# Kernel tuning notes

Hardware: AMD Instinct MI355X
Metric: run time of the kernel (lower is better)

The kernel has to match this reference:

```python
import jax, jax.numpy as jnp
import numpy as np

WIN = 7
NUM_HEADS = 4
DIM = 128
HEAD_DIM = DIM // NUM_HEADS
N = WIN * WIN
NW = 1024   # windows per image (224/7)^2
B_ = 16384  # batch(16) * NW


def _pos_index(win):
    # Swin relative-position index, static int table [N, N]
    coords = np.stack(np.meshgrid(np.arange(win), np.arange(win), indexing='ij'))
    cf = coords.reshape(2, -1)                       # [2, N]
    rel = cf[:, :, None] - cf[:, None, :]            # [2, N, N]
    rel = rel.transpose(1, 2, 0).astype(np.int64)    # [N, N, 2]
    rel[:, :, 0] += win - 1
    rel[:, :, 1] += win - 1
    rel[:, :, 0] *= 2 * win - 1
    return rel.sum(-1)                               # [N, N]

POS_INDEX = jnp.asarray(_pos_index(WIN))


def setup_inputs() -> dict:
    key = jax.random.key(0)
    ks = jax.random.split(key, 11)
    s = 0.02
    return {
        'x': jax.random.normal(ks[0], (B_, N, DIM), jnp.float32),
        'mask': jax.random.normal(ks[1], (NW, N, N), jnp.float32),
        'Wq': jax.random.normal(ks[2], (DIM, DIM), jnp.float32) * s,
        'bq': jax.random.normal(ks[3], (DIM,), jnp.float32) * s,
        'Wk': jax.random.normal(ks[4], (DIM, DIM), jnp.float32) * s,
        'bk': jax.random.normal(ks[5], (DIM,), jnp.float32) * s,
        'Wv': jax.random.normal(ks[6], (DIM, DIM), jnp.float32) * s,
        'bv': jax.random.normal(ks[7], (DIM,), jnp.float32) * s,
        'Wproj': jax.random.normal(ks[8], (DIM, DIM), jnp.float32) * s,
        'bproj': jax.random.normal(ks[9], (DIM,), jnp.float32) * s,
        'rel_bias': jax.random.normal(ks[10], ((2 * WIN - 1) ** 2, NUM_HEADS), jnp.float32) * s,
    }


def reference(x, mask, Wq, bq, Wk, bk, Wv, bv, Wproj, bproj, rel_bias):
    Bw, n, C = x.shape
    H, hd = NUM_HEADS, HEAD_DIM
    scale = hd ** -0.5

    def heads(t):  # [B, N, C] -> [B, H, N, hd]
        return t.reshape(Bw, n, H, hd).transpose(0, 2, 1, 3)

    q = heads(x @ Wq.T + bq) * scale
    k = heads(x @ Wk.T + bk)
    v = heads(x @ Wv.T + bv)

    attn = jnp.einsum('bhnd,bhmd->bhnm', q, k)              # [B, H, N, N]
    rb = rel_bias[POS_INDEX.reshape(-1)].reshape(n, n, H)    # [N, N, H]
    attn = attn + rb.transpose(2, 0, 1)[None]                # + [1, H, N, N]

    nw = mask.shape[0]
    attn = attn.reshape(Bw // nw, nw, H, n, n) + mask[None, :, None]
    attn = attn.reshape(Bw, H, n, n)

    attn = jax.nn.softmax(attn, axis=-1)
    out = jnp.einsum('bhnm,bhmd->bhnd', attn, v)             # [B, H, N, hd]
    out = out.transpose(0, 2, 1, 3).reshape(Bw, n, C)
    return out @ Wproj.T + bproj
```

## Files before the change

### kernel.cpp

```cpp
#include <hip/hip_runtime.h>
#include <hip/hip_bf16.h>
#include <stdint.h>

#define NTOK 49
#define LOG2E 1.4426950408889634f
#define SCALE2 0.25507662683243807f

typedef __attribute__((ext_vector_type(4))) float f32x4;
typedef __attribute__((ext_vector_type(2))) unsigned int u32x2;
typedef __attribute__((ext_vector_type(4))) unsigned int u32x4;
typedef __attribute__((ext_vector_type(8))) short bfrag;
typedef __attribute__((ext_vector_type(4))) short s16x4;
typedef __attribute__((ext_vector_type(4))) float facc;

#define MFMA16(A,B,C) __builtin_amdgcn_mfma_f32_16x16x32_bf16(A,B,C,0,0,0)
#define EXP2(x) __builtin_amdgcn_exp2f(x)

__device__ __forceinline__ unsigned pk2bf(float a, float b) {
    unsigned r;
    asm("v_cvt_pk_bf16_f32 %0, %1, %2" : "=v"(r) : "v"(a), "v"(b));
    return r;
}
__device__ __forceinline__ short f2bf(float a) {
    unsigned ua = __builtin_bit_cast(unsigned, a);
    ua = ua + 0x7fffu + ((ua >> 16) & 1u);
    return (short)(ua >> 16);
}
__device__ __forceinline__ float bf2f(short s) {
    unsigned u = ((unsigned)(unsigned short)s) << 16;
    return __builtin_bit_cast(float, u);
}
__device__ __forceinline__ int sw256(int row, int cb) { return row * 256 + (cb ^ ((row & 7) << 4)); }
__device__ __forceinline__ int sw128(int row, int cb) { return row * 128 + (cb ^ ((row & 7) << 4)); }

__global__ void prep_w(const float* __restrict__ Wq, const float* __restrict__ Wk,
                       const float* __restrict__ Wv, const float* __restrict__ Wp,
                       const float* __restrict__ relb, short* __restrict__ ws)
{
    int t = blockIdx.x * 256 + threadIdx.x;
    if (t >= 16384) return;
    int e = t & 7, lane = (t >> 3) & 63, ks = (t >> 9) & 3, tile = t >> 11;
    int row = tile * 16 + (lane & 15);
    int col = ks * 32 + (lane >> 4) * 8 + e;
    int src = row * 128 + col;
    ws[t]         = f2bf(Wq[src]);
    ws[16384 + t] = f2bf(Wk[src]);
    ws[32768 + t] = f2bf(Wv[src]);
    ws[49152 + t] = f2bf(Wp[src]);
    int e2 = t & 3, lane2 = (t >> 2) & 63, mt = (t >> 8) & 3, rt = (t >> 10) & 3, h = t >> 12;
    int r = rt * 16 + (lane2 & 15);
    int m = mt * 16 + (lane2 >> 4) * 4 + e2;
    float v = 0.f;
    if (r < NTOK && m < NTOK) {
        int idx = ((r / 7 - m / 7) + 6) * 13 + ((r % 7) - (m % 7) + 6);
        v = relb[idx * 4 + h] * LOG2E;
    }
    ws[65536 + t] = f2bf(v);
}

__global__ void prep_cmb(const float* __restrict__ mask, const float* __restrict__ relb,
                         short* __restrict__ cmb)
{
    int t = blockIdx.x * 256 + threadIdx.x;
    int e = t & 3, lane = (t >> 2) & 63, mt = (t >> 8) & 3, rt = (t >> 10) & 3;
    int h = (t >> 12) & 3, w = t >> 14;
    int r = rt * 16 + (lane & 15);
    int m = mt * 16 + (lane >> 4) * 4 + e;
    float v = -1e30f;
    if (r < NTOK && m < NTOK) {
        int idx = ((r / 7 - m / 7) + 6) * 13 + ((r % 7) - (m % 7) + 6);
        v = (mask[w * (NTOK * NTOK) + r * NTOK + m] + relb[idx * 4 + h]) * LOG2E;
    }
    cmb[t] = f2bf(v);
}

__device__ __forceinline__ char* pstrip(char* smem_, int wid, int r, int mb) {
    return smem_ + ((mb >> 6) << 14) + r * 256 + ((wid * 64 + (mb & 63)) ^ ((r & 7) << 4));
}

__global__ __launch_bounds__(256, 2) void swin_fwd_p(
    const float* __restrict__ x,
    const float* __restrict__ bq, const float* __restrict__ bk,
    const float* __restrict__ bv, const float* __restrict__ bp,
    const short* __restrict__ wqf, const short* __restrict__ wkf,
    const short* __restrict__ wvf, const short* __restrict__ wpf,
    const short* __restrict__ cmbf, float* __restrict__ out)
{
    extern __shared__ char smem[];
    char* qbuf  = smem;
    char* kbuf  = smem + 16384;
    char* vtbuf = smem + 32768;
    char* r4    = smem + 49152;

    const int b = blockIdx.x;
    const int tid = threadIdx.x;
    const int wid = tid >> 6;
    const int lane = tid & 63;
    const int l16 = lane & 15;
    const int lg = lane >> 4;

    float bqv[2][4], bkv[2][4], bpv[2][4], bvv2[2];
    #pragma unroll
    for (int mt = 0; mt < 2; ++mt) {
        #pragma unroll
        for (int j = 0; j < 4; ++j) {
            int o = wid * 32 + mt * 16 + lg * 4 + j;
            bqv[mt][j] = bq[o]; bkv[mt][j] = bk[o]; bpv[mt][j] = bp[o];
        }
        bvv2[mt] = bv[wid * 32 + mt * 16 + l16];
    }

    bfrag aq[2][4], ak[2][4], av[2][4];
    {
        const short* wq_i = wqf; const short* wk_i = wkf; const short* wv_i = wvf;
        asm volatile("" : "+s"(wq_i), "+s"(wk_i), "+s"(wv_i));
        #pragma unroll
        for (int mt = 0; mt < 2; ++mt)
            #pragma unroll
            for (int ks = 0; ks < 4; ++ks) {
                int fi = (((wid * 2 + mt) * 4 + ks) * 64 + lane) * 8;
                aq[mt][ks] = *(const bfrag*)(wq_i + fi);
                ak[mt][ks] = *(const bfrag*)(wk_i + fi);
                av[mt][ks] = *(const bfrag*)(wv_i + fi);
            }
    }

    f32x4 xr[7];
    {
        const float* xw0 = x + (size_t)b * 6272;
        #pragma unroll
        for (int ii = 0; ii < 7; ++ii) {
            int i4 = ii * 256 + tid;
            if (i4 < 1568) xr[ii] = *(const f32x4*)(xw0 + i4 * 4);
        }
        #pragma unroll
        for (int ii = 0; ii < 7; ++ii) {
            int i4 = ii * 256 + tid;
            if (i4 < 1568) {
                int tok = i4 >> 5, col = (i4 & 31) * 4;
                u32x2 w; w.x = pk2bf(xr[ii].x, xr[ii].y); w.y = pk2bf(xr[ii].z, xr[ii].w);
                *(u32x2*)(r4 + sw256(tok, col * 2)) = w;
            }
        }
        if (tid < 240) { u32x4 z = {0, 0, 0, 0}; *(u32x4*)(r4 + 49 * 256 + tid * 16) = z; }
    }
    __syncthreads();

    #pragma unroll 1
    for (int it = 0; it < 32; ++it) {
        const int win = b + (it << 9);

        {
            const float* xn = x + (size_t)((win + 512) & 16383) * 6272;
            #pragma unroll
            for (int ii = 0; ii < 7; ++ii) {
                int i4 = ii * 256 + tid;
                if (i4 < 1568) xr[ii] = *(const f32x4*)(xn + i4 * 4);
            }
        }

        {
            #pragma unroll
            for (int nt = 0; nt < 4; ++nt) {
                bfrag bx[4];
                #pragma unroll
                for (int ks = 0; ks < 4; ++ks)
                    bx[ks] = *(const bfrag*)(r4 + sw256(nt * 16 + l16, (ks * 32 + lg * 8) * 2));
                facc accq[2] = {{0,0,0,0},{0,0,0,0}};
                facc acck[2] = {{0,0,0,0},{0,0,0,0}};
                facc accv[2] = {{0,0,0,0},{0,0,0,0}};
                __builtin_amdgcn_s_setprio(1);
                #pragma unroll
                for (int ks = 0; ks < 4; ++ks)
                    #pragma unroll
                    for (int mt = 0; mt < 2; ++mt) {
                        accq[mt] = MFMA16(aq[mt][ks], bx[ks], accq[mt]);
                        acck[mt] = MFMA16(ak[mt][ks], bx[ks], acck[mt]);
                        accv[mt] = MFMA16(bx[ks], av[mt][ks], accv[mt]);
                    }
                __builtin_amdgcn_s_setprio(0);
                int tok = nt * 16 + l16;
                #pragma unroll
                for (int mt = 0; mt < 2; ++mt) {
                    int o0 = wid * 32 + mt * 16 + lg * 4;
                    u32x2 wq2, wk2, wv2;
                    wq2.x = pk2bf((accq[mt][0] + bqv[mt][0]) * SCALE2, (accq[mt][1] + bqv[mt][1]) * SCALE2);
                    wq2.y = pk2bf((accq[mt][2] + bqv[mt][2]) * SCALE2, (accq[mt][3] + bqv[mt][3]) * SCALE2);
                    wk2.x = pk2bf(acck[mt][0] + bkv[mt][0], acck[mt][1] + bkv[mt][1]);
                    wk2.y = pk2bf(acck[mt][2] + bkv[mt][2], acck[mt][3] + bkv[mt][3]);
                    *(u32x2*)(qbuf + sw256(tok, o0 * 2)) = wq2;
                    *(u32x2*)(kbuf + sw256(tok, o0 * 2)) = wk2;
                    wv2.x = pk2bf(accv[mt][0] + bvv2[mt], accv[mt][1] + bvv2[mt]);
                    wv2.y = pk2bf(accv[mt][2] + bvv2[mt], accv[mt][3] + bvv2[mt]);
                    *(u32x2*)(vtbuf + sw128(wid * 32 + mt * 16 + l16, (nt * 16 + lg * 4) * 2)) = wv2;
                }
            }
        }

        facc s[4][4];
        {
            bfrag ka[4], qb[4];
            int cb = (wid * 32 + lg * 8) * 2;
            #pragma unroll
            for (int t = 0; t < 4; ++t) {
                ka[t] = *(const bfrag*)(kbuf + sw256(t * 16 + l16, cb));
                qb[t] = *(const bfrag*)(qbuf + sw256(t * 16 + l16, cb));
            }
            __builtin_amdgcn_s_setprio(1);
            #pragma unroll
            for (int mt = 0; mt < 4; ++mt)
                #pragma unroll
                for (int rt = 0; rt < 4; ++rt) {
                    facc z = {0, 0, 0, 0};
                    s[mt][rt] = MFMA16(ka[mt], qb[rt], z);
                }
            __builtin_amdgcn_s_setprio(0);
        }
        __syncthreads();

        {
            #pragma unroll
            for (int ii = 0; ii < 7; ++ii) {
                int i4 = ii * 256 + tid;
                if (i4 < 1568) {
                    int tok = i4 >> 5, col = (i4 & 31) * 4;
                    u32x2 w; w.x = pk2bf(xr[ii].x, xr[ii].y); w.y = pk2bf(xr[ii].z, xr[ii].w);
                    *(u32x2*)(r4 + sw256(tok, col * 2)) = w;
                }
            }
        }

        float rs4[4];
        {
            const short* cw = cmbf + ((size_t)((win & 1023) * 4 + wid) << 12);
            #pragma unroll
            for (int rt = 0; rt < 4; ++rt) {
                float lgt[4][4];
                float mx = -3e38f;
                #pragma unroll
                for (int mt = 0; mt < 4; ++mt) {
                    s16x4 b4 = *(const s16x4*)(cw + ((rt * 4 + mt) << 8) + lane * 4);
                    #pragma unroll
                    for (int j = 0; j < 4; ++j) {
                        float v = s[mt][rt][j] + bf2f(b4[j]);
                        lgt[mt][j] = v;
                        mx = fmaxf(mx, v);
                    }
                }
                mx = fmaxf(mx, __shfl_xor(mx, 16));
                mx = fmaxf(mx, __shfl_xor(mx, 32));
                float sum = 0.f;
                u32x2 pw[4];
                #pragma unroll
                for (int mt = 0; mt < 4; ++mt) {
                    float p0 = EXP2(lgt[mt][0] - mx);
                    float p1 = EXP2(lgt[mt][1] - mx);
                    float p2 = EXP2(lgt[mt][2] - mx);
                    float p3 = EXP2(lgt[mt][3] - mx);
                    sum += (p0 + p1) + (p2 + p3);
                    pw[mt].x = pk2bf(p0, p1);
                    pw[mt].y = pk2bf(p2, p3);
                }
                sum += __shfl_xor(sum, 16);
                sum += __shfl_xor(sum, 32);
                rs4[rt] = __builtin_amdgcn_rcpf(sum);
                int r = rt * 16 + l16;
                #pragma unroll
                for (int mt = 0; mt < 4; ++mt)
                    *(u32x2*)pstrip(smem, wid, r, mt * 32 + lg * 8) = pw[mt];
            }
        }

        facc o2[2][4];
        {
            #pragma unroll
            for (int ct = 0; ct < 2; ++ct)
                #pragma unroll
                for (int rt = 0; rt < 4; ++rt) o2[ct][rt] = (facc){0, 0, 0, 0};
            #pragma unroll
            for (int ks = 0; ks < 2; ++ks) {
                bfrag avf[2], pb[4];
                #pragma unroll
                for (int ct = 0; ct < 2; ++ct)
                    avf[ct] = *(const bfrag*)(vtbuf + sw128(wid * 32 + ct * 16 + l16, (ks * 32 + lg * 8) * 2));
                #pragma unroll
                for (int rt = 0; rt < 4; ++rt)
                    pb[rt] = *(const bfrag*)pstrip(smem, wid, rt * 16 + l16, ks * 64 + lg * 16);
                __builtin_amdgcn_s_setprio(1);
                #pragma unroll
                for (int ct = 0; ct < 2; ++ct)
                    #pragma unroll
                    for (int rt = 0; rt < 4; ++rt)
                        o2[ct][rt] = MFMA16(avf[ct], pb[rt], o2[ct][rt]);
                __builtin_amdgcn_s_setprio(0);
            }
        }
        bfrag ap[2][4];
        {
            const short* wp_i = wpf;
            asm volatile("" : "+s"(wp_i));
            #pragma unroll
            for (int mt = 0; mt < 2; ++mt)
                #pragma unroll
                for (int ks = 0; ks < 4; ++ks)
                    ap[mt][ks] = *(const bfrag*)(wp_i + (((wid * 2 + mt) * 4 + ks) * 64 + lane) * 8);
        }
        __syncthreads();
        {
            #pragma unroll
            for (int ct = 0; ct < 2; ++ct) {
                int c0 = wid * 32 + ct * 16 + lg * 4;
                #pragma unroll
                for (int rt = 0; rt < 4; ++rt) {
                    int r = rt * 16 + l16;
                    float sc = rs4[rt];
                    u32x2 w;
                    w.x = pk2bf(o2[ct][rt][0] * sc, o2[ct][rt][1] * sc);
                    w.y = pk2bf(o2[ct][rt][2] * sc, o2[ct][rt][3] * sc);
                    *(u32x2*)(qbuf + sw256(r, c0 * 2)) = w;
                }
            }
        }
        __syncthreads();

        {
            facc acco[2][4];
            #pragma unroll
            for (int mt = 0; mt < 2; ++mt)
                #pragma unroll
                for (int tt = 0; tt < 4; ++tt) acco[mt][tt] = (facc){0, 0, 0, 0};
            #pragma unroll
            for (int tt = 0; tt < 4; ++tt) {
                bfrag ba[4];
                #pragma unroll
                for (int ks = 0; ks < 4; ++ks)
                    ba[ks] = *(const bfrag*)(qbuf + sw256(tt * 16 + l16, (ks * 32 + lg * 8) * 2));
                __builtin_amdgcn_s_setprio(1);
                #pragma unroll
                for (int ks = 0; ks < 4; ++ks)
                    #pragma unroll
                    for (int mt = 0; mt < 2; ++mt)
                        acco[mt][tt] = MFMA16(ap[mt][ks], ba[ks], acco[mt][tt]);
                __builtin_amdgcn_s_setprio(0);
            }
            float* ow = out + (size_t)win * 6272;
            #pragma unroll
            for (int tt = 0; tt < 4; ++tt) {
                int tok = tt * 16 + l16;
                if (tok < NTOK) {
                    #pragma unroll
                    for (int mt = 0; mt < 2; ++mt) {
                        int o0 = wid * 32 + mt * 16 + lg * 4;
                        f32x4 w;
                        w.x = acco[mt][tt][0] + bpv[mt][0];
                        w.y = acco[mt][tt][1] + bpv[mt][1];
                        w.z = acco[mt][tt][2] + bpv[mt][2];
                        w.w = acco[mt][tt][3] + bpv[mt][3];
                        *(f32x4*)(ow + tok * 128 + o0) = w;
                    }
                }
            }
        }

        {
            const short* wq_i = wqf; const short* wk_i = wkf; const short* wv_i = wvf;
            asm volatile("" : "+s"(wq_i), "+s"(wk_i), "+s"(wv_i));
            #pragma unroll
            for (int mt = 0; mt < 2; ++mt)
                #pragma unroll
                for (int ks = 0; ks < 4; ++ks) {
                    int fi = (((wid * 2 + mt) * 4 + ks) * 64 + lane) * 8;
                    aq[mt][ks] = *(const bfrag*)(wq_i + fi);
                    ak[mt][ks] = *(const bfrag*)(wk_i + fi);
                    av[mt][ks] = *(const bfrag*)(wv_i + fi);
                }
        }
        __syncthreads();
    }
}

__global__ __launch_bounds__(256, 2) void swin_fwd_fb(
    const float* __restrict__ x, const float* __restrict__ mask,
    const float* __restrict__ bq, const float* __restrict__ bk,
    const float* __restrict__ bv, const float* __restrict__ bp,
    const short* __restrict__ wqf, const short* __restrict__ wkf,
    const short* __restrict__ wvf, const short* __restrict__ wpf,
    const short* __restrict__ rbf, float* __restrict__ out)
{
    extern __shared__ char smem[];
    char* qbuf  = smem;
    char* kbuf  = smem + 16384;
    char* vtbuf = smem + 32768;
    char* r4    = smem + 49152;

    const int win = blockIdx.x;
    const int tid = threadIdx.x;
    const int wid = tid >> 6;
    const int lane = tid & 63;
    const int l16 = lane & 15;
    const int lg = lane >> 4;

    {
        const float* xw = x + (size_t)win * 6272;
        #pragma unroll
        for (int i = 0; i < 7; ++i) {
            int i4 = i * 256 + tid;
            if (i4 < 1568) {
                f32x4 f = *(const f32x4*)(xw + i4 * 4);
                int tok = i4 >> 5, col = (i4 & 31) * 4;
                u32x2 w; w.x = pk2bf(f.x, f.y); w.y = pk2bf(f.z, f.w);
                *(u32x2*)(r4 + sw256(tok, col * 2)) = w;
            }
        }
        if (tid < 240) { u32x4 z = {0, 0, 0, 0}; *(u32x4*)(r4 + 49 * 256 + tid * 16) = z; }
    }
    bfrag aq[2][4], ak[2][4], av[2][4];
    float bqv[2][4], bkv[2][4], bvv2[2];
    #pragma unroll
    for (int mt = 0; mt < 2; ++mt) {
        #pragma unroll
        for (int ks = 0; ks < 4; ++ks) {
            int fi = (((wid * 2 + mt) * 4 + ks) * 64 + lane) * 8;
            aq[mt][ks] = *(const bfrag*)(wqf + fi);
            ak[mt][ks] = *(const bfrag*)(wkf + fi);
            av[mt][ks] = *(const bfrag*)(wvf + fi);
        }
        #pragma unroll
        for (int j = 0; j < 4; ++j) {
            int o = wid * 32 + mt * 16 + lg * 4 + j;
            bqv[mt][j] = bq[o]; bkv[mt][j] = bk[o];
        }
        bvv2[mt] = bv[wid * 32 + mt * 16 + l16];
    }
    __syncthreads();

    {
        #pragma unroll
        for (int nt = 0; nt < 4; ++nt) {
            bfrag bx[4];
            #pragma unroll
            for (int ks = 0; ks < 4; ++ks)
                bx[ks] = *(const bfrag*)(r4 + sw256(nt * 16 + l16, (ks * 32 + lg * 8) * 2));
            facc accq[2] = {{0,0,0,0},{0,0,0,0}};
            facc acck[2] = {{0,0,0,0},{0,0,0,0}};
            facc accv[2] = {{0,0,0,0},{0,0,0,0}};
            #pragma unroll
            for (int ks = 0; ks < 4; ++ks)
                #pragma unroll
                for (int mt = 0; mt < 2; ++mt) {
                    accq[mt] = MFMA16(aq[mt][ks], bx[ks], accq[mt]);
                    acck[mt] = MFMA16(ak[mt][ks], bx[ks], acck[mt]);
                    accv[mt] = MFMA16(bx[ks], av[mt][ks], accv[mt]);
                }
            int tok = nt * 16 + l16;
            #pragma unroll
            for (int mt = 0; mt < 2; ++mt) {
                int o0 = wid * 32 + mt * 16 + lg * 4;
                u32x2 wq2, wk2, wv2;
                wq2.x = pk2bf((accq[mt][0] + bqv[mt][0]) * SCALE2, (accq[mt][1] + bqv[mt][1]) * SCALE2);
                wq2.y = pk2bf((accq[mt][2] + bqv[mt][2]) * SCALE2, (accq[mt][3] + bqv[mt][3]) * SCALE2);
                wk2.x = pk2bf(acck[mt][0] + bkv[mt][0], acck[mt][1] + bkv[mt][1]);
                wk2.y = pk2bf(acck[mt][2] + bkv[mt][2], acck[mt][3] + bkv[mt][3]);
                *(u32x2*)(qbuf + sw256(tok, o0 * 2)) = wq2;
                *(u32x2*)(kbuf + sw256(tok, o0 * 2)) = wk2;
                wv2.x = pk2bf(accv[mt][0] + bvv2[mt], accv[mt][1] + bvv2[mt]);
                wv2.y = pk2bf(accv[mt][2] + bvv2[mt], accv[mt][3] + bvv2[mt]);
                *(u32x2*)(vtbuf + sw128(wid * 32 + mt * 16 + l16, (nt * 16 + lg * 4) * 2)) = wv2;
            }
        }
    }
    facc s[4][4];
    {
        bfrag ka[4], qb[4];
        int cb = (wid * 32 + lg * 8) * 2;
        #pragma unroll
        for (int t = 0; t < 4; ++t) {
            ka[t] = *(const bfrag*)(kbuf + sw256(t * 16 + l16, cb));
            qb[t] = *(const bfrag*)(qbuf + sw256(t * 16 + l16, cb));
        }
        #pragma unroll
        for (int mt = 0; mt < 4; ++mt)
            #pragma unroll
            for (int rt = 0; rt < 4; ++rt) {
                facc z = {0, 0, 0, 0};
                s[mt][rt] = MFMA16(ka[mt], qb[rt], z);
            }
    }
    __syncthreads();
    {
        const float* mw = mask + (size_t)(win & 1023) * (NTOK * NTOK);
        #pragma unroll
        for (int i = 0; i < 16; ++i) {
            int flat = i * 256 + tid;
            int r = flat >> 6, m = flat & 63;
            float v = -1e30f;
            if (r < NTOK && m < NTOK) v = mw[r * 49 + m] * LOG2E;
            *(float*)(r4 + sw256(r, m * 4)) = v;
        }
    }
    __syncthreads();
    float rs4[4];
    {
        #pragma unroll
        for (int rt = 0; rt < 4; ++rt) {
            int r = rt * 16 + l16;
            float lgt[4][4];
            float mx = -3e38f;
            #pragma unroll
            for (int mt = 0; mt < 4; ++mt) {
                s16x4 b4 = *(const s16x4*)(rbf + ((wid * 16 + rt * 4 + mt) * 64 + lane) * 4);
                f32x4 mk = *(const f32x4*)(r4 + sw256(r, (mt * 16 + lg * 4) * 4));
                #pragma unroll
                for (int j = 0; j < 4; ++j) {
                    float v = s[mt][rt][j] + bf2f(b4[j]) + mk[j];
                    lgt[mt][j] = v;
                    mx = fmaxf(mx, v);
                }
            }
            mx = fmaxf(mx, __shfl_xor(mx, 16));
            mx = fmaxf(mx, __shfl_xor(mx, 32));
            float sum = 0.f;
            u32x2 pw[4];
            #pragma unroll
            for (int mt = 0; mt < 4; ++mt) {
                float p0 = EXP2(lgt[mt][0] - mx);
                float p1 = EXP2(lgt[mt][1] - mx);
                float p2 = EXP2(lgt[mt][2] - mx);
                float p3 = EXP2(lgt[mt][3] - mx);
                sum += (p0 + p1) + (p2 + p3);
                pw[mt].x = pk2bf(p0, p1);
                pw[mt].y = pk2bf(p2, p3);
            }
            sum += __shfl_xor(sum, 16);
            sum += __shfl_xor(sum, 32);
            rs4[rt] = __builtin_amdgcn_rcpf(sum);
            #pragma unroll
            for (int mt = 0; mt < 4; ++mt)
                *(u32x2*)pstrip(smem, wid, r, mt * 32 + lg * 8) = pw[mt];
        }
    }
    facc o2[2][4];
    {
        #pragma unroll
        for (int ct = 0; ct < 2; ++ct)
            #pragma unroll
            for (int rt = 0; rt < 4; ++rt) o2[ct][rt] = (facc){0, 0, 0, 0};
        #pragma unroll
        for (int ks = 0; ks < 2; ++ks) {
            bfrag avf[2], pb[4];
            #pragma unroll
            for (int ct = 0; ct < 2; ++ct)
                avf[ct] = *(const bfrag*)(vtbuf + sw128(wid * 32 + ct * 16 + l16, (ks * 32 + lg * 8) * 2));
            #pragma unroll
            for (int rt = 0; rt < 4; ++rt)
                pb[rt] = *(const bfrag*)pstrip(smem, wid, rt * 16 + l16, ks * 64 + lg * 16);
            #pragma unroll
            for (int ct = 0; ct < 2; ++ct)
                #pragma unroll
                for (int rt = 0; rt < 4; ++rt)
                    o2[ct][rt] = MFMA16(avf[ct], pb[rt], o2[ct][rt]);
        }
    }
    bfrag ap[2][4];
    float bpv[2][4];
    #pragma unroll
    for (int mt = 0; mt < 2; ++mt) {
        #pragma unroll
        for (int ks = 0; ks < 4; ++ks)
            ap[mt][ks] = *(const bfrag*)(wpf + (((wid * 2 + mt) * 4 + ks) * 64 + lane) * 8);
        #pragma unroll
        for (int j = 0; j < 4; ++j)
            bpv[mt][j] = bp[wid * 32 + mt * 16 + lg * 4 + j];
    }
    __syncthreads();
    {
        #pragma unroll
        for (int ct = 0; ct < 2; ++ct) {
            int c0 = wid * 32 + ct * 16 + lg * 4;
            #pragma unroll
            for (int rt = 0; rt < 4; ++rt) {
                int r = rt * 16 + l16;
                float sc = rs4[rt];
                u32x2 w;
                w.x = pk2bf(o2[ct][rt][0] * sc, o2[ct][rt][1] * sc);
                w.y = pk2bf(o2[ct][rt][2] * sc, o2[ct][rt][3] * sc);
                *(u32x2*)(r4 + sw256(r, c0 * 2)) = w;
            }
        }
    }
    __syncthreads();
    {
        facc acco[2][4];
        #pragma unroll
        for (int mt = 0; mt < 2; ++mt)
            #pragma unroll
            for (int tt = 0; tt < 4; ++tt) acco[mt][tt] = (facc){0, 0, 0, 0};
        #pragma unroll
        for (int tt = 0; tt < 4; ++tt) {
            bfrag ba[4];
            #pragma unroll
            for (int ks = 0; ks < 4; ++ks)
                ba[ks] = *(const bfrag*)(r4 + sw256(tt * 16 + l16, (ks * 32 + lg * 8) * 2));
            #pragma unroll
            for (int ks = 0; ks < 4; ++ks)
                #pragma unroll
                for (int mt = 0; mt < 2; ++mt)
                    acco[mt][tt] = MFMA16(ap[mt][ks], ba[ks], acco[mt][tt]);
        }
        float* ow = out + (size_t)win * 6272;
        #pragma unroll
        for (int tt = 0; tt < 4; ++tt) {
            int tok = tt * 16 + l16;
            if (tok < NTOK) {
                #pragma unroll
                for (int mt = 0; mt < 2; ++mt) {
                    int o0 = wid * 32 + mt * 16 + lg * 4;
                    f32x4 w;
                    w.x = acco[mt][tt][0] + bpv[mt][0];
                    w.y = acco[mt][tt][1] + bpv[mt][1];
                    w.z = acco[mt][tt][2] + bpv[mt][2];
                    w.w = acco[mt][tt][3] + bpv[mt][3];
                    *(f32x4*)(ow + tok * 128 + o0) = w;
                }
            }
        }
    }
}

extern "C" void kernel_launch(void* const* d_in, const int* in_sizes, int n_in,
                              void* d_out, int out_size, void* d_ws, size_t ws_size,
                              hipStream_t stream)
{
    const float* x    = (const float*)d_in[0];
    const float* mask = (const float*)d_in[1];
    const float* Wq   = (const float*)d_in[2];
    const float* bq   = (const float*)d_in[3];
    const float* Wk   = (const float*)d_in[4];
    const float* bk   = (const float*)d_in[5];
    const float* Wv   = (const float*)d_in[6];
    const float* bv   = (const float*)d_in[7];
    const float* Wp   = (const float*)d_in[8];
    const float* bp   = (const float*)d_in[9];
    const float* rlb  = (const float*)d_in[10];
    short* ws = (short*)d_ws;
    short* cmb = ws + 81920;
    const size_t need = ((size_t)81920 + (size_t)16777216) * 2;
    const bool use_cmb = ws_size >= need;

    prep_w<<<64, 256, 0, stream>>>(Wq, Wk, Wv, Wp, rlb, ws);
    if (use_cmb) {
        prep_cmb<<<65536, 256, 0, stream>>>(mask, rlb, cmb);
        swin_fwd_p<<<512, 256, 65536, stream>>>(x, bq, bk, bv, bp,
            ws, ws + 16384, ws + 32768, ws + 49152, cmb, (float*)d_out);
    } else {
        swin_fwd_fb<<<16384, 256, 65536, stream>>>(x, mask, bq, bk, bv, bp,
            ws, ws + 16384, ws + 32768, ws + 49152, ws + 65536, (float*)d_out);
    }
}
```

Baseline: 370.6 us.

## Split persistent Swin window kernel across 8 waves with per-head token halves

```diff
diff --git a/kernel.cpp b/kernel.cpp
--- a/kernel.cpp
+++ b/kernel.cpp
@@ -15,6 +15,7 @@
 
 #define MFMA16(A,B,C) __builtin_amdgcn_mfma_f32_16x16x32_bf16(A,B,C,0,0,0)
 #define EXP2(x) __builtin_amdgcn_exp2f(x)
+#define MEMBAR() asm volatile("" ::: "memory")
 
 __device__ __forceinline__ unsigned pk2bf(float a, float b) {
     unsigned r;
@@ -31,7 +32,10 @@
     return __builtin_bit_cast(float, u);
 }
 __device__ __forceinline__ int sw256(int row, int cb) { return row * 256 + (cb ^ ((row & 7) << 4)); }
-__device__ __forceinline__ int sw128(int row, int cb) { return row * 128 + (cb ^ ((row & 7) << 4)); }
+__device__ __forceinline__ int sw128v(int row, int cb) { return row * 128 + (cb ^ ((row & 7) << 4)); }
+__device__ __forceinline__ char* pstrip(char* smem_, int h, int r, int mb) {
+    return smem_ + ((mb >> 6) << 14) + r * 256 + ((h * 64 + (mb & 63)) ^ ((r & 7) << 4));
+}
 
 __global__ void prep_w(const float* __restrict__ Wq, const float* __restrict__ Wk,
                        const float* __restrict__ Wv, const float* __restrict__ Wp,
@@ -74,11 +78,7 @@
     cmb[t] = f2bf(v);
 }
 
-__device__ __forceinline__ char* pstrip(char* smem_, int wid, int r, int mb) {
-    return smem_ + ((mb >> 6) << 14) + r * 256 + ((wid * 64 + (mb & 63)) ^ ((r & 7) << 4));
-}
-
-__global__ __launch_bounds__(256, 2) void swin_fwd_p(
+__global__ __launch_bounds__(512, 4) void swin_fwd_p(
     const float* __restrict__ x,
     const float* __restrict__ bq, const float* __restrict__ bk,
     const float* __restrict__ bv, const float* __restrict__ bp,
@@ -86,7 +86,7 @@
     const short* __restrict__ wvf, const short* __restrict__ wpf,
     const short* __restrict__ cmbf, float* __restrict__ out)
 {
-    extern __shared__ char smem[];
+    __shared__ __align__(16) char smem[65536];
     char* qbuf  = smem;
     char* kbuf  = smem + 16384;
     char* vtbuf = smem + 32768;
@@ -95,50 +95,37 @@
     const int b = blockIdx.x;
     const int tid = threadIdx.x;
     const int wid = tid >> 6;
+    const int h = wid & 3;
+    const int u = wid >> 2;
     const int lane = tid & 63;
     const int l16 = lane & 15;
     const int lg = lane >> 4;
 
-    float bqv[2][4], bkv[2][4], bpv[2][4], bvv2[2];
+    float bqv[2][4], bkv[2][4], bvv2[2];
     #pragma unroll
     for (int mt = 0; mt < 2; ++mt) {
         #pragma unroll
         for (int j = 0; j < 4; ++j) {
-            int o = wid * 32 + mt * 16 + lg * 4 + j;
-            bqv[mt][j] = bq[o]; bkv[mt][j] = bk[o]; bpv[mt][j] = bp[o];
-        }
-        bvv2[mt] = bv[wid * 32 + mt * 16 + l16];
-    }
-
-    bfrag aq[2][4], ak[2][4], av[2][4];
-    {
-        const short* wq_i = wqf; const short* wk_i = wkf; const short* wv_i = wvf;
-        asm volatile("" : "+s"(wq_i), "+s"(wk_i), "+s"(wv_i));
-        #pragma unroll
-        for (int mt = 0; mt < 2; ++mt)
-            #pragma unroll
-            for (int ks = 0; ks < 4; ++ks) {
-                int fi = (((wid * 2 + mt) * 4 + ks) * 64 + lane) * 8;
-                aq[mt][ks] = *(const bfrag*)(wq_i + fi);
-                ak[mt][ks] = *(const bfrag*)(wk_i + fi);
-                av[mt][ks] = *(const bfrag*)(wv_i + fi);
-            }
-    }
-
-    f32x4 xr[7];
-    {
+            int o = h * 32 + mt * 16 + lg * 4 + j;
+            bqv[mt][j] = bq[o]; bkv[mt][j] = bk[o];
+        }
+        bvv2[mt] = bv[h * 32 + mt * 16 + l16];
+    }
+
+    {
+        f32x4 xp[4];
         const float* xw0 = x + (size_t)b * 6272;
         #pragma unroll
-        for (int ii = 0; ii < 7; ++ii) {
-            int i4 = ii * 256 + tid;
-            if (i4 < 1568) xr[ii] = *(const f32x4*)(xw0 + i4 * 4);
-        }
-        #pragma unroll
-        for (int ii = 0; ii < 7; ++ii) {
-            int i4 = ii * 256 + tid;
+        for (int ii = 0; ii < 4; ++ii) {
+            int i4 = ii * 512 + tid;
+            if (i4 < 1568) xp[ii] = *(const f32x4*)(xw0 + i4 * 4);
+        }
+        #pragma unroll
+        for (int ii = 0; ii < 4; ++ii) {
+            int i4 = ii * 512 + tid;
             if (i4 < 1568) {
                 int tok = i4 >> 5, col = (i4 & 31) * 4;
-                u32x2 w; w.x = pk2bf(xr[ii].x, xr[ii].y); w.y = pk2bf(xr[ii].z, xr[ii].w);
+                u32x2 w; w.x = pk2bf(xp[ii].x, xp[ii].y); w.y = pk2bf(xp[ii].z, xp[ii].w);
                 *(u32x2*)(r4 + sw256(tok, col * 2)) = w;
             }
         }
@@ -151,24 +138,63 @@
         const int win = b + (it << 9);
 
         {
-            const float* xn = x + (size_t)((win + 512) & 16383) * 6272;
-            #pragma unroll
-            for (int ii = 0; ii < 7; ++ii) {
-                int i4 = ii * 256 + tid;
-                if (i4 < 1568) xr[ii] = *(const f32x4*)(xn + i4 * 4);
-            }
-        }
-
+            bfrag av[2][4];
+            {
+                const short* wv_i = wvf;
+                asm volatile("" : "+s"(wv_i));
+                #pragma unroll
+                for (int mt = 0; mt < 2; ++mt)
+                    #pragma unroll
+                    for (int ks = 0; ks < 4; ++ks)
+                        av[mt][ks] = *(const bfrag*)(wv_i + (((h * 2 + mt) * 4 + ks) * 64 + lane) * 8);
+            }
+            #pragma unroll
+            for (int nt2 = 0; nt2 < 2; ++nt2) {
+                int nt = u * 2 + nt2;
+                bfrag bx[4];
+                #pragma unroll
+                for (int ks = 0; ks < 4; ++ks)
+                    bx[ks] = *(const bfrag*)(r4 + sw256(nt * 16 + l16, (ks * 32 + lg * 8) * 2));
+                facc accv[2] = {{0,0,0,0},{0,0,0,0}};
+                __builtin_amdgcn_s_setprio(1);
+                #pragma unroll
+                for (int ks = 0; ks < 4; ++ks)
+                    #pragma unroll
+                    for (int mt = 0; mt < 2; ++mt)
+                        accv[mt] = MFMA16(bx[ks], av[mt][ks], accv[mt]);
+                __builtin_amdgcn_s_setprio(0);
+                #pragma unroll
+                for (int mt = 0; mt < 2; ++mt) {
+                    u32x2 wv2;
+                    wv2.x = pk2bf(accv[mt][0] + bvv2[mt], accv[mt][1] + bvv2[mt]);
+                    wv2.y = pk2bf(accv[mt][2] + bvv2[mt], accv[mt][3] + bvv2[mt]);
+                    *(u32x2*)(vtbuf + sw128v(h * 32 + mt * 16 + l16, (nt * 16 + lg * 4) * 2)) = wv2;
+                }
+            }
+        }
         {
-            #pragma unroll
-            for (int nt = 0; nt < 4; ++nt) {
+            bfrag aq[2][4], ak[2][4];
+            {
+                const short* wq_i = wqf; const short* wk_i = wkf;
+                asm volatile("" : "+s"(wq_i), "+s"(wk_i));
+                #pragma unroll
+                for (int mt = 0; mt < 2; ++mt)
+                    #pragma unroll
+                    for (int ks = 0; ks < 4; ++ks) {
+                        int fi = (((h * 2 + mt) * 4 + ks) * 64 + lane) * 8;
+                        aq[mt][ks] = *(const bfrag*)(wq_i + fi);
+                        ak[mt][ks] = *(const bfrag*)(wk_i + fi);
+                    }
+            }
+            #pragma unroll
+            for (int nt2 = 0; nt2 < 2; ++nt2) {
+                int nt = u * 2 + nt2;
                 bfrag bx[4];
                 #pragma unroll
                 for (int ks = 0; ks < 4; ++ks)
                     bx[ks] = *(const bfrag*)(r4 + sw256(nt * 16 + l16, (ks * 32 + lg * 8) * 2));
                 facc accq[2] = {{0,0,0,0},{0,0,0,0}};
                 facc acck[2] = {{0,0,0,0},{0,0,0,0}};
-                facc accv[2] = {{0,0,0,0},{0,0,0,0}};
                 __builtin_amdgcn_s_setprio(1);
                 #pragma unroll
                 for (int ks = 0; ks < 4; ++ks)
@@ -176,52 +202,107 @@
                     for (int mt = 0; mt < 2; ++mt) {
                         accq[mt] = MFMA16(aq[mt][ks], bx[ks], accq[mt]);
                         acck[mt] = MFMA16(ak[mt][ks], bx[ks], acck[mt]);
-                        accv[mt] = MFMA16(bx[ks], av[mt][ks], accv[mt]);
                     }
                 __builtin_amdgcn_s_setprio(0);
                 int tok = nt * 16 + l16;
                 #pragma unroll
                 for (int mt = 0; mt < 2; ++mt) {
-                    int o0 = wid * 32 + mt * 16 + lg * 4;
-                    u32x2 wq2, wk2, wv2;
+                    int cb = (h * 32 + mt * 16 + lg * 4) * 2;
+                    u32x2 wq2, wk2;
                     wq2.x = pk2bf((accq[mt][0] + bqv[mt][0]) * SCALE2, (accq[mt][1] + bqv[mt][1]) * SCALE2);
                     wq2.y = pk2bf((accq[mt][2] + bqv[mt][2]) * SCALE2, (accq[mt][3] + bqv[mt][3]) * SCALE2);
                     wk2.x = pk2bf(acck[mt][0] + bkv[mt][0], acck[mt][1] + bkv[mt][1]);
                     wk2.y = pk2bf(acck[mt][2] + bkv[mt][2], acck[mt][3] + bkv[mt][3]);
-                    *(u32x2*)(qbuf + sw256(tok, o0 * 2)) = wq2;
-                    *(u32x2*)(kbuf + sw256(tok, o0 * 2)) = wk2;
-                    wv2.x = pk2bf(accv[mt][0] + bvv2[mt], accv[mt][1] + bvv2[mt]);
-                    wv2.y = pk2bf(accv[mt][2] + bvv2[mt], accv[mt][3] + bvv2[mt]);
-                    *(u32x2*)(vtbuf + sw128(wid * 32 + mt * 16 + l16, (nt * 16 + lg * 4) * 2)) = wv2;
-                }
-            }
-        }
-
-        facc s[4][4];
+                    *(u32x2*)(qbuf + sw256(tok, cb)) = wq2;
+                    *(u32x2*)(kbuf + sw256(tok, cb)) = wk2;
+                }
+            }
+        }
+        __syncthreads();
+
+        f32x4 xr[4];
+        if (it + 1 < 32) {
+            const float* xn = x + (size_t)(win + 512) * 6272;
+            #pragma unroll
+            for (int ii = 0; ii < 4; ++ii) {
+                int i4 = ii * 512 + tid;
+                if (i4 < 1568) xr[ii] = *(const f32x4*)(xn + i4 * 4);
+            }
+        }
+
+        bfrag ka[4], qb[2];
         {
-            bfrag ka[4], qb[4];
-            int cb = (wid * 32 + lg * 8) * 2;
-            #pragma unroll
-            for (int t = 0; t < 4; ++t) {
+            int cb = (h * 32 + lg * 8) * 2;
+            #pragma unroll
+            for (int t = 0; t < 4; ++t)
                 ka[t] = *(const bfrag*)(kbuf + sw256(t * 16 + l16, cb));
-                qb[t] = *(const bfrag*)(qbuf + sw256(t * 16 + l16, cb));
-            }
+            #pragma unroll
+            for (int rt2 = 0; rt2 < 2; ++rt2)
+                qb[rt2] = *(const bfrag*)(qbuf + sw256((u * 2 + rt2) * 16 + l16, cb));
+        }
+        s16x4 b4r[2][4];
+        {
+            const short* cw = cmbf + ((size_t)((win & 1023) * 4 + h) << 12);
+            #pragma unroll
+            for (int rt2 = 0; rt2 < 2; ++rt2)
+                #pragma unroll
+                for (int mt = 0; mt < 4; ++mt)
+                    b4r[rt2][mt] = *(const s16x4*)(cw + (((u * 2 + rt2) * 4 + mt) << 8) + lane * 4);
+        }
+
+        facc s[4][2];
+        {
             __builtin_amdgcn_s_setprio(1);
             #pragma unroll
             for (int mt = 0; mt < 4; ++mt)
                 #pragma unroll
-                for (int rt = 0; rt < 4; ++rt) {
+                for (int rt2 = 0; rt2 < 2; ++rt2) {
                     facc z = {0, 0, 0, 0};
-                    s[mt][rt] = MFMA16(ka[mt], qb[rt], z);
+                    s[mt][rt2] = MFMA16(ka[mt], qb[rt2], z);
                 }
             __builtin_amdgcn_s_setprio(0);
         }
         __syncthreads();
 
-        {
-            #pragma unroll
-            for (int ii = 0; ii < 7; ++ii) {
-                int i4 = ii * 256 + tid;
+        float rs2[2];
+        #pragma unroll
+        for (int rt2 = 0; rt2 < 2; ++rt2) {
+            int r = (u * 2 + rt2) * 16 + l16;
+            float lgt[4][4];
+            float mx = -3e38f;
+            #pragma unroll
+            for (int mt = 0; mt < 4; ++mt)
+                #pragma unroll
+                for (int j = 0; j < 4; ++j) {
+                    float v = s[mt][rt2][j] + bf2f(b4r[rt2][mt][j]);
+                    lgt[mt][j] = v;
+                    mx = fmaxf(mx, v);
+                }
+            mx = fmaxf(mx, __shfl_xor(mx, 16));
+            mx = fmaxf(mx, __shfl_xor(mx, 32));
+            float sum = 0.f;
+            u32x2 pw[4];
+            #pragma unroll
+            for (int mt = 0; mt < 4; ++mt) {
+                float p0 = EXP2(lgt[mt][0] - mx);
+                float p1 = EXP2(lgt[mt][1] - mx);
+                float p2 = EXP2(lgt[mt][2] - mx);
+                float p3 = EXP2(lgt[mt][3] - mx);
+                sum += (p0 + p1) + (p2 + p3);
+                pw[mt].x = pk2bf(p0, p1);
+                pw[mt].y = pk2bf(p2, p3);
+            }
+            sum += __shfl_xor(sum, 16);
+            sum += __shfl_xor(sum, 32);
+            rs2[rt2] = __builtin_amdgcn_rcpf(sum);
+            #pragma unroll
+            for (int mt = 0; mt < 4; ++mt)
+                *(u32x2*)pstrip(smem, h, r, mt * 32 + lg * 8) = pw[mt];
+        }
+        if (it + 1 < 32) {
+            #pragma unroll
+            for (int ii = 0; ii < 4; ++ii) {
+                int i4 = ii * 512 + tid;
                 if (i4 < 1568) {
                     int tok = i4 >> 5, col = (i4 & 31) * 4;
                     u32x2 w; w.x = pk2bf(xr[ii].x, xr[ii].y); w.y = pk2bf(xr[ii].z, xr[ii].w);
@@ -229,108 +310,73 @@
                 }
             }
         }
-
-        float rs4[4];
-        {
-            const short* cw = cmbf + ((size_t)((win & 1023) * 4 + wid) << 12);
-            #pragma unroll
-            for (int rt = 0; rt < 4; ++rt) {
-                float lgt[4][4];
-                float mx = -3e38f;
-                #pragma unroll
-                for (int mt = 0; mt < 4; ++mt) {
-                    s16x4 b4 = *(const s16x4*)(cw + ((rt * 4 + mt) << 8) + lane * 4);
-                    #pragma unroll
-                    for (int j = 0; j < 4; ++j) {
-                        float v = s[mt][rt][j] + bf2f(b4[j]);
-                        lgt[mt][j] = v;
-                        mx = fmaxf(mx, v);
-                    }
-                }
-                mx = fmaxf(mx, __shfl_xor(mx, 16));
-                mx = fmaxf(mx, __shfl_xor(mx, 32));
-                float sum = 0.f;
-                u32x2 pw[4];
-                #pragma unroll
-                for (int mt = 0; mt < 4; ++mt) {
-                    float p0 = EXP2(lgt[mt][0] - mx);
-                    float p1 = EXP2(lgt[mt][1] - mx);
-                    float p2 = EXP2(lgt[mt][2] - mx);
-                    float p3 = EXP2(lgt[mt][3] - mx);
-                    sum += (p0 + p1) + (p2 + p3);
-                    pw[mt].x = pk2bf(p0, p1);
-                    pw[mt].y = pk2bf(p2, p3);
-                }
-                sum += __shfl_xor(sum, 16);
-                sum += __shfl_xor(sum, 32);
-                rs4[rt] = __builtin_amdgcn_rcpf(sum);
-                int r = rt * 16 + l16;
-                #pragma unroll
-                for (int mt = 0; mt < 4; ++mt)
-                    *(u32x2*)pstrip(smem, wid, r, mt * 32 + lg * 8) = pw[mt];
-            }
-        }
-
-        facc o2[2][4];
-        {
+        MEMBAR();
+
+        facc o2[2][2];
+        #pragma unroll
+        for (int ct = 0; ct < 2; ++ct)
+            #pragma unroll
+            for (int rt2 = 0; rt2 < 2; ++rt2) o2[ct][rt2] = (facc){0, 0, 0, 0};
+        #pragma unroll
+        for (int ks = 0; ks < 2; ++ks) {
+            bfrag avf[2], pb[2];
             #pragma unroll
             for (int ct = 0; ct < 2; ++ct)
-                #pragma unroll
-                for (int rt = 0; rt < 4; ++rt) o2[ct][rt] = (facc){0, 0, 0, 0};
-            #pragma unroll
-            for (int ks = 0; ks < 2; ++ks) {
-                bfrag avf[2], pb[4];
-                #pragma unroll
-                for (int ct = 0; ct < 2; ++ct)
-                    avf[ct] = *(const bfrag*)(vtbuf + sw128(wid * 32 + ct * 16 + l16, (ks * 32 + lg * 8) * 2));
-                #pragma unroll
-                for (int rt = 0; rt < 4; ++rt)
-                    pb[rt] = *(const bfrag*)pstrip(smem, wid, rt * 16 + l16, ks * 64 + lg * 16);
-                __builtin_amdgcn_s_setprio(1);
-                #pragma unroll
-                for (int ct = 0; ct < 2; ++ct)
-                    #pragma unroll
-                    for (int rt = 0; rt < 4; ++rt)
-                        o2[ct][rt] = MFMA16(avf[ct], pb[rt], o2[ct][rt]);
-                __builtin_amdgcn_s_setprio(0);
-            }
-        }
+                avf[ct] = *(const bfrag*)(vtbuf + sw128v(h * 32 + ct * 16 + l16, (ks * 32 + lg * 8) * 2));
+            #pragma unroll
+            for (int rt2 = 0; rt2 < 2; ++rt2)
+                pb[rt2] = *(const bfrag*)pstrip(smem, h, (u * 2 + rt2) * 16 + l16, ks * 64 + lg * 16);
+            __builtin_amdgcn_s_setprio(1);
+            #pragma unroll
+            for (int ct = 0; ct < 2; ++ct)
+                #pragma unroll
+                for (int rt2 = 0; rt2 < 2; ++rt2)
+                    o2[ct][rt2] = MFMA16(avf[ct], pb[rt2], o2[ct][rt2]);
+            __builtin_amdgcn_s_setprio(0);
+        }
+        u32x2 attw[2][2];
+        #pragma unroll
+        for (int ct = 0; ct < 2; ++ct)
+            #pragma unroll
+            for (int rt2 = 0; rt2 < 2; ++rt2) {
+                float sc = rs2[rt2];
+                attw[ct][rt2].x = pk2bf(o2[ct][rt2][0] * sc, o2[ct][rt2][1] * sc);
+                attw[ct][rt2].y = pk2bf(o2[ct][rt2][2] * sc, o2[ct][rt2][3] * sc);
+            }
         bfrag ap[2][4];
+        float bpv[2][4];
         {
             const short* wp_i = wpf;
             asm volatile("" : "+s"(wp_i));
             #pragma unroll
+            for (int mt = 0; mt < 2; ++mt) {
+                #pragma unroll
+                for (int ks = 0; ks < 4; ++ks)
+                    ap[mt][ks] = *(const bfrag*)(wp_i + (((h * 2 + mt) * 4 + ks) * 64 + lane) * 8);
+                #pragma unroll
+                for (int j = 0; j < 4; ++j)
+                    bpv[mt][j] = bp[h * 32 + mt * 16 + lg * 4 + j];
+            }
+        }
+        __syncthreads();
+        #pragma unroll
+        for (int ct = 0; ct < 2; ++ct)
+            #pragma unroll
+            for (int rt2 = 0; rt2 < 2; ++rt2) {
+                int r = (u * 2 + rt2) * 16 + l16;
+                *(u32x2*)(qbuf + sw256(r, (h * 32 + ct * 16 + lg * 4) * 2)) = attw[ct][rt2];
+            }
+        __syncthreads();
+
+        {
+            facc acco[2][2];
+            #pragma unroll
             for (int mt = 0; mt < 2; ++mt)
                 #pragma unroll
-                for (int ks = 0; ks < 4; ++ks)
-                    ap[mt][ks] = *(const bfrag*)(wp_i + (((wid * 2 + mt) * 4 + ks) * 64 + lane) * 8);
-        }
-        __syncthreads();
-        {
-            #pragma unroll
-            for (int ct = 0; ct < 2; ++ct) {
-                int c0 = wid * 32 + ct * 16 + lg * 4;
-                #pragma unroll
-                for (int rt = 0; rt < 4; ++rt) {
-                    int r = rt * 16 + l16;
-                    float sc = rs4[rt];
-                    u32x2 w;
-                    w.x = pk2bf(o2[ct][rt][0] * sc, o2[ct][rt][1] * sc);
-                    w.y = pk2bf(o2[ct][rt][2] * sc, o2[ct][rt][3] * sc);
-                    *(u32x2*)(qbuf + sw256(r, c0 * 2)) = w;
-                }
-            }
-        }
-        __syncthreads();
-
-        {
-            facc acco[2][4];
-            #pragma unroll
-            for (int mt = 0; mt < 2; ++mt)
-                #pragma unroll
-                for (int tt = 0; tt < 4; ++tt) acco[mt][tt] = (facc){0, 0, 0, 0};
-            #pragma unroll
-            for (int tt = 0; tt < 4; ++tt) {
+                for (int tt2 = 0; tt2 < 2; ++tt2) acco[mt][tt2] = (facc){0, 0, 0, 0};
+            #pragma unroll
+            for (int tt2 = 0; tt2 < 2; ++tt2) {
+                int tt = u * 2 + tt2;
                 bfrag ba[4];
                 #pragma unroll
                 for (int ks = 0; ks < 4; ++ks)
@@ -340,40 +386,26 @@
                 for (int ks = 0; ks < 4; ++ks)
                     #pragma unroll
                     for (int mt = 0; mt < 2; ++mt)
-                        acco[mt][tt] = MFMA16(ap[mt][ks], ba[ks], acco[mt][tt]);
+                        acco[mt][tt2] = MFMA16(ap[mt][ks], ba[ks], acco[mt][tt2]);
                 __builtin_amdgcn_s_setprio(0);
             }
             float* ow = out + (size_t)win * 6272;
             #pragma unroll
-            for (int tt = 0; tt < 4; ++tt) {
-                int tok = tt * 16 + l16;
+            for (int tt2 = 0; tt2 < 2; ++tt2) {
+                int tok = (u * 2 + tt2) * 16 + l16;
                 if (tok < NTOK) {
                     #pragma unroll
                     for (int mt = 0; mt < 2; ++mt) {
-                        int o0 = wid * 32 + mt * 16 + lg * 4;
+                        int o0 = h * 32 + mt * 16 + lg * 4;
                         f32x4 w;
-                        w.x = acco[mt][tt][0] + bpv[mt][0];
-                        w.y = acco[mt][tt][1] + bpv[mt][1];
-                        w.z = acco[mt][tt][2] + bpv[mt][2];
-                        w.w = acco[mt][tt][3] + bpv[mt][3];
+                        w.x = acco[mt][tt2][0] + bpv[mt][0];
+                        w.y = acco[mt][tt2][1] + bpv[mt][1];
+                        w.z = acco[mt][tt2][2] + bpv[mt][2];
+                        w.w = acco[mt][tt2][3] + bpv[mt][3];
                         *(f32x4*)(ow + tok * 128 + o0) = w;
                     }
                 }
             }
-        }
-
-        {
-            const short* wq_i = wqf; const short* wk_i = wkf; const short* wv_i = wvf;
-            asm volatile("" : "+s"(wq_i), "+s"(wk_i), "+s"(wv_i));
-            #pragma unroll
-            for (int mt = 0; mt < 2; ++mt)
-                #pragma unroll
-                for (int ks = 0; ks < 4; ++ks) {
-                    int fi = (((wid * 2 + mt) * 4 + ks) * 64 + lane) * 8;
-                    aq[mt][ks] = *(const bfrag*)(wq_i + fi);
-                    ak[mt][ks] = *(const bfrag*)(wk_i + fi);
-                    av[mt][ks] = *(const bfrag*)(wv_i + fi);
-                }
         }
         __syncthreads();
     }
@@ -387,11 +419,11 @@
     const short* __restrict__ wvf, const short* __restrict__ wpf,
     const short* __restrict__ rbf, float* __restrict__ out)
 {
-    extern __shared__ char smem[];
-    char* qbuf  = smem;
-    char* kbuf  = smem + 16384;
-    char* vtbuf = smem + 32768;
-    char* r4    = smem + 49152;
+    extern __shared__ char dsm[];
+    char* qbuf  = dsm;
+    char* kbuf  = dsm + 16384;
+    char* vtbuf = dsm + 32768;
+    char* r4    = dsm + 49152;
 
     const int win = blockIdx.x;
     const int tid = threadIdx.x;
@@ -465,10 +497,11 @@
                 *(u32x2*)(kbuf + sw256(tok, o0 * 2)) = wk2;
                 wv2.x = pk2bf(accv[mt][0] + bvv2[mt], accv[mt][1] + bvv2[mt]);
                 wv2.y = pk2bf(accv[mt][2] + bvv2[mt], accv[mt][3] + bvv2[mt]);
-                *(u32x2*)(vtbuf + sw128(wid * 32 + mt * 16 + l16, (nt * 16 + lg * 4) * 2)) = wv2;
-            }
-        }
-    }
+                *(u32x2*)(vtbuf + sw128v(wid * 32 + mt * 16 + l16, (nt * 16 + lg * 4) * 2)) = wv2;
+            }
+        }
+    }
+    MEMBAR();
     facc s[4][4];
     {
         bfrag ka[4], qb[4];
@@ -536,9 +569,10 @@
             rs4[rt] = __builtin_amdgcn_rcpf(sum);
             #pragma unroll
             for (int mt = 0; mt < 4; ++mt)
-                *(u32x2*)pstrip(smem, wid, r, mt * 32 + lg * 8) = pw[mt];
-        }
-    }
+                *(u32x2*)pstrip(dsm, wid, r, mt * 32 + lg * 8) = pw[mt];
+        }
+    }
+    MEMBAR();
     facc o2[2][4];
     {
         #pragma unroll
@@ -550,10 +584,10 @@
             bfrag avf[2], pb[4];
             #pragma unroll
             for (int ct = 0; ct < 2; ++ct)
-                avf[ct] = *(const bfrag*)(vtbuf + sw128(wid * 32 + ct * 16 + l16, (ks * 32 + lg * 8) * 2));
+                avf[ct] = *(const bfrag*)(vtbuf + sw128v(wid * 32 + ct * 16 + l16, (ks * 32 + lg * 8) * 2));
             #pragma unroll
             for (int rt = 0; rt < 4; ++rt)
-                pb[rt] = *(const bfrag*)pstrip(smem, wid, rt * 16 + l16, ks * 64 + lg * 16);
+                pb[rt] = *(const bfrag*)pstrip(dsm, wid, rt * 16 + l16, ks * 64 + lg * 16);
             #pragma unroll
             for (int ct = 0; ct < 2; ++ct)
                 #pragma unroll
@@ -650,7 +684,7 @@
     prep_w<<<64, 256, 0, stream>>>(Wq, Wk, Wv, Wp, rlb, ws);
     if (use_cmb) {
         prep_cmb<<<65536, 256, 0, stream>>>(mask, rlb, cmb);
-        swin_fwd_p<<<512, 256, 65536, stream>>>(x, bq, bk, bv, bp,
+        swin_fwd_p<<<512, 512, 0, stream>>>(x, bq, bk, bv, bp,
             ws, ws + 16384, ws + 32768, ws + 49152, cmb, (float*)d_out);
     } else {
         swin_fwd_fb<<<16384, 256, 65536, stream>>>(x, mask, bq, bk, bv, bp,
```

Result: slower. 759.1 us (+104.8%).
